# Optimization experiments

Hardware: AMD Instinct MI355X
Metric: run time of the kernel (lower is better)

Reference implementation:

```python
import jax, jax.numpy as jnp
import numpy as np

M, K, N, P = 2048, 4096, 64, 16   # prev outputs, decoder nodes, matrix size, parents per node
ACTIVE_THRESHOLD = 12             # >= 12/16 active parents required

def setup_inputs() -> dict:
    key = jax.random.key(0)
    k1, k2, k3, k4, k5 = jax.random.split(key, 5)
    prev_outputs = jax.random.normal(k1, (M, N, N), dtype=jnp.float32)
    prev_is_active = jax.random.bernoulli(k2, 0.9, (M,))                 # bool (M,)
    parent_indices = jax.random.randint(k3, (K, P), 0, M)                # static wiring (K,16)
    w = jax.random.normal(k4, (K, P), dtype=jnp.float32) / np.sqrt(P)    # per-node parent weights
    b = jax.random.normal(k5, (K,), dtype=jnp.float32) * 0.01            # per-node bias
    return {"prev_outputs": prev_outputs, "prev_is_active": prev_is_active,
            "parent_indices": parent_indices, "w": w, "b": b}

def reference(prev_outputs, prev_is_active, parent_indices, w, b):
    # gather parent outputs: (K, P, n, n)
    gathered = prev_outputs[parent_indices]
    # per-node decoder: weighted combine of 16 parents + bias, tanh
    combined = jnp.einsum('kp,kpnm->knm', w, gathered) + b[:, None, None]
    out = jnp.tanh(combined)[:, None]                                    # (K,1,n,n)
    # activity threshold gate: node active iff >= 12 of 16 parents active
    n_active = prev_is_active[parent_indices].astype(jnp.int32).sum(axis=-1)  # (K,)
    out_active = n_active >= ACTIVE_THRESHOLD
    out = jnp.where(out_active[:, None, None, None], out, jnp.zeros_like(out))
    return out, out_active
```

## Files before the change

### kernel.cpp

```cpp
#include <hip/hip_runtime.h>


#define M_ROWS   2048
#define K_NODES  4096
#define NN       4096
#define POS_TILE 16
#define NTHREADS 1024
#define ROW_B    48
#define LDS_BYTES (M_ROWS * ROW_B)
#define OUT_ELEMS (K_NODES * NN)
#define ACTIVE_THRESHOLD 12

typedef float f32x4 __attribute__((ext_vector_type(4)));
typedef unsigned short u16x8 __attribute__((ext_vector_type(8)));

__device__ __forceinline__ float fast_tanh(float x) {
  float ax = __builtin_fabsf(x);
  float e  = __expf(-2.0f * ax);
  float r  = (1.0f - e) * __builtin_amdgcn_rcpf(1.0f + e);
  return __builtin_copysignf(r, x);
}

__device__ __forceinline__ unsigned short f2bf_rne(float f) {
  unsigned u = __float_as_uint(f);
  u += 0x7FFFu + ((u >> 16) & 1u);
  return (unsigned short)(u >> 16);
}

__global__ __launch_bounds__(256) void act_kernel(
    const int* __restrict__ pidx, const unsigned int* __restrict__ isact,
    float* __restrict__ outact) {
  __shared__ int mode_sh;
  if (threadIdx.x == 0) mode_sh = 0;
  __syncthreads();
  int bad = 0;
  for (int i = threadIdx.x; i < 512; i += 256) bad |= (isact[i] > 1u);
  if (bad) atomicOr(&mode_sh, 1);
  __syncthreads();
  const int shift = mode_sh ? 0 : 2;
  const unsigned char* actb = (const unsigned char*)isact;

  int k = blockIdx.x * 256 + threadIdx.x;
  const int4* ip = (const int4*)(pidx + k * 16);
  int4 ia = ip[0], ib = ip[1], ic = ip[2], id4 = ip[3];
  int ids[16] = {ia.x, ia.y, ia.z, ia.w, ib.x, ib.y, ib.z, ib.w,
                 ic.x, ic.y, ic.z, ic.w, id4.x, id4.y, id4.z, id4.w};
  int n = 0;
  #pragma unroll
  for (int p = 0; p < 16; ++p) n += (actb[ids[p] << shift] != 0);
  outact[k] = (n >= ACTIVE_THRESHOLD) ? 1.0f : 0.0f;
}

#define PFMA(vv, wv)                                              \
  { float wv_ = (wv);                                             \
    a0 += wv_ * __uint_as_float((unsigned)(vv)[0] << 16);         \
    a1 += wv_ * __uint_as_float((unsigned)(vv)[1] << 16);         \
    a2 += wv_ * __uint_as_float((unsigned)(vv)[2] << 16);         \
    a3 += wv_ * __uint_as_float((unsigned)(vv)[3] << 16);         \
    a4 += wv_ * __uint_as_float((unsigned)(vv)[4] << 16);         \
    a5 += wv_ * __uint_as_float((unsigned)(vv)[5] << 16);         \
    a6 += wv_ * __uint_as_float((unsigned)(vv)[6] << 16);         \
    a7 += wv_ * __uint_as_float((unsigned)(vv)[7] << 16); }

__global__ __launch_bounds__(NTHREADS, 1) void decoder_kernel(
    const float* __restrict__ prev, const int* __restrict__ pidx,
    const float* __restrict__ w, const float* __restrict__ b,
    const float* __restrict__ actf, float* __restrict__ out,
    float* __restrict__ outact) {
  extern __shared__ char xb[];
  const int tid  = threadIdx.x;
  const int bid  = blockIdx.x;
  const int pos0 = bid * POS_TILE;

  #pragma unroll
  for (int it = 0; it < 4; ++it) {
    int ci = (it << 10) + tid;
    int r = ci >> 1, c = ci & 1;
    const float* sp = prev + r * NN + pos0 + (c << 3);
    f32x4 v0 = *(const f32x4*)sp;
    f32x4 v1 = *(const f32x4*)(sp + 4);
    u16x8 o;
    o[0] = f2bf_rne(v0.x); o[1] = f2bf_rne(v0.y);
    o[2] = f2bf_rne(v0.z); o[3] = f2bf_rne(v0.w);
    o[4] = f2bf_rne(v1.x); o[5] = f2bf_rne(v1.y);
    o[6] = f2bf_rne(v1.z); o[7] = f2bf_rne(v1.w);
    *(u16x8*)(xb + r * ROW_B + (c << 4)) = o;
  }
  __syncthreads();

  const int q  = tid & 1;
  const int s  = tid >> 1;
  const int qb = q << 4;

  for (int it = 0; it < 8; ++it) {
    int n = (it << 9) + s;
    const int4*   ip = (const int4*)(pidx + (n << 4));
    const float4* wp = (const float4*)(w + (n << 4));
    int4   i0 = ip[0], i1 = ip[1], i2 = ip[2], i3 = ip[3];
    float4 w0 = wp[0], w1 = wp[1], w2 = wp[2], w3 = wp[3];
    float  bk = b[n];
    float  g  = actf[n];

    float a0 = bk, a1 = bk, a2 = bk, a3 = bk;
    float a4 = bk, a5 = bk, a6 = bk, a7 = bk;

    u16x8 v0 = *(const u16x8*)(xb + i0.x * ROW_B + qb);
    u16x8 v1 = *(const u16x8*)(xb + i0.y * ROW_B + qb);
    u16x8 v2 = *(const u16x8*)(xb + i0.z * ROW_B + qb);
    u16x8 v3 = *(const u16x8*)(xb + i0.w * ROW_B + qb);
    u16x8 v4 = *(const u16x8*)(xb + i1.x * ROW_B + qb);
    u16x8 v5 = *(const u16x8*)(xb + i1.y * ROW_B + qb);
    u16x8 v6 = *(const u16x8*)(xb + i1.z * ROW_B + qb);
    u16x8 v7 = *(const u16x8*)(xb + i1.w * ROW_B + qb);
    __builtin_amdgcn_sched_barrier(0);
    PFMA(v0, w0.x) PFMA(v1, w0.y) PFMA(v2, w0.z) PFMA(v3, w0.w)
    PFMA(v4, w1.x) PFMA(v5, w1.y) PFMA(v6, w1.z) PFMA(v7, w1.w)

    v0 = *(const u16x8*)(xb + i2.x * ROW_B + qb);
    v1 = *(const u16x8*)(xb + i2.y * ROW_B + qb);
    v2 = *(const u16x8*)(xb + i2.z * ROW_B + qb);
    v3 = *(const u16x8*)(xb + i2.w * ROW_B + qb);
    v4 = *(const u16x8*)(xb + i3.x * ROW_B + qb);
    v5 = *(const u16x8*)(xb + i3.y * ROW_B + qb);
    v6 = *(const u16x8*)(xb + i3.z * ROW_B + qb);
    v7 = *(const u16x8*)(xb + i3.w * ROW_B + qb);
    __builtin_amdgcn_sched_barrier(0);
    PFMA(v0, w2.x) PFMA(v1, w2.y) PFMA(v2, w2.z) PFMA(v3, w2.w)
    PFMA(v4, w3.x) PFMA(v5, w3.y) PFMA(v6, w3.z) PFMA(v7, w3.w)

    f32x4 o0, o1;
    o0.x = fast_tanh(a0) * g; o0.y = fast_tanh(a1) * g;
    o0.z = fast_tanh(a2) * g; o0.w = fast_tanh(a3) * g;
    o1.x = fast_tanh(a4) * g; o1.y = fast_tanh(a5) * g;
    o1.z = fast_tanh(a6) * g; o1.w = fast_tanh(a7) * g;

    float* op = out + ((size_t)n << 12) + pos0 + (q << 3);
    *(f32x4*)op       = o0;
    *(f32x4*)(op + 4) = o1;

    if (bid == 0 && q == 0) outact[n] = g;
  }
}

extern "C" void kernel_launch(void* const* d_in, const int* in_sizes, int n_in,
                              void* d_out, int out_size, void* d_ws, size_t ws_size,
                              hipStream_t stream) {
  const float* prev  = (const float*)d_in[0];
  const void*  isact = d_in[1];
  const int*   pidx  = (const int*)d_in[2];
  const float* w     = (const float*)d_in[3];
  const float* b     = (const float*)d_in[4];
  float* out    = (float*)d_out;
  float* outact = out + OUT_ELEMS;

  (void)hipFuncSetAttribute((const void*)decoder_kernel,
                            hipFuncAttributeMaxDynamicSharedMemorySize, LDS_BYTES);

  act_kernel<<<K_NODES / 256, 256, 0, stream>>>(
      pidx, (const unsigned int*)isact, outact);
  decoder_kernel<<<NN / POS_TILE, NTHREADS, LDS_BYTES, stream>>>(
      prev, pidx, w, b, outact, out, outact);
}
```

Baseline: 41.15 us.

## Halve position tile, one node per thread, XCD-aware block remap

Shrinks the per-block position tile from 16 to 8, so the bf16 LDS staging buffer drops to 24-byte rows (48 KB) and each thread handles a whole node's 8 positions instead of two threads sharing a node. Launch bounds now request multiple blocks per CU to raise occupancy, and block ids are remapped so consecutive tiles land on the same XCD for L2 locality of prev reads. The redundant outact write from block 0 is removed. In exchange the grid doubles, pidx and w are re-read by twice as many blocks, and LDS reads become two 8-byte loads per parent row, which may hit more bank conflicts.

```diff
diff --git a/kernel.cpp b/kernel.cpp
--- a/kernel.cpp
+++ b/kernel.cpp
@@ -4,15 +4,15 @@
 #define M_ROWS   2048
 #define K_NODES  4096
 #define NN       4096
-#define POS_TILE 16
+#define POS_TILE 8
 #define NTHREADS 1024
-#define ROW_B    48
+#define ROW_B    24
 #define LDS_BYTES (M_ROWS * ROW_B)
 #define OUT_ELEMS (K_NODES * NN)
 #define ACTIVE_THRESHOLD 12
 
 typedef float f32x4 __attribute__((ext_vector_type(4)));
-typedef unsigned short u16x8 __attribute__((ext_vector_type(8)));
+typedef unsigned short u16x4 __attribute__((ext_vector_type(4)));
 
 __device__ __forceinline__ float fast_tanh(float x) {
   float ax = __builtin_fabsf(x);
@@ -51,49 +51,48 @@
   outact[k] = (n >= ACTIVE_THRESHOLD) ? 1.0f : 0.0f;
 }
 
-#define PFMA(vv, wv)                                              \
-  { float wv_ = (wv);                                             \
-    a0 += wv_ * __uint_as_float((unsigned)(vv)[0] << 16);         \
-    a1 += wv_ * __uint_as_float((unsigned)(vv)[1] << 16);         \
-    a2 += wv_ * __uint_as_float((unsigned)(vv)[2] << 16);         \
-    a3 += wv_ * __uint_as_float((unsigned)(vv)[3] << 16);         \
-    a4 += wv_ * __uint_as_float((unsigned)(vv)[4] << 16);         \
-    a5 += wv_ * __uint_as_float((unsigned)(vv)[5] << 16);         \
-    a6 += wv_ * __uint_as_float((unsigned)(vv)[6] << 16);         \
-    a7 += wv_ * __uint_as_float((unsigned)(vv)[7] << 16); }
+#define PFMA2(lo, hi, wv)                                          \
+  { float wv_ = (wv);                                              \
+    a0 += wv_ * __uint_as_float((unsigned)(lo)[0] << 16);          \
+    a1 += wv_ * __uint_as_float((unsigned)(lo)[1] << 16);          \
+    a2 += wv_ * __uint_as_float((unsigned)(lo)[2] << 16);          \
+    a3 += wv_ * __uint_as_float((unsigned)(lo)[3] << 16);          \
+    a4 += wv_ * __uint_as_float((unsigned)(hi)[0] << 16);          \
+    a5 += wv_ * __uint_as_float((unsigned)(hi)[1] << 16);          \
+    a6 += wv_ * __uint_as_float((unsigned)(hi)[2] << 16);          \
+    a7 += wv_ * __uint_as_float((unsigned)(hi)[3] << 16); }
 
-__global__ __launch_bounds__(NTHREADS, 1) void decoder_kernel(
+__global__ __launch_bounds__(NTHREADS, 8) void decoder_kernel(
     const float* __restrict__ prev, const int* __restrict__ pidx,
     const float* __restrict__ w, const float* __restrict__ b,
-    const float* __restrict__ actf, float* __restrict__ out,
-    float* __restrict__ outact) {
+    const float* __restrict__ actf, float* __restrict__ out) {
   extern __shared__ char xb[];
-  const int tid  = threadIdx.x;
-  const int bid  = blockIdx.x;
-  const int pos0 = bid * POS_TILE;
+  const int tid = threadIdx.x;
+  const int bid = blockIdx.x;
+
+  const int xcd  = bid & 7;
+  const int tile = xcd * 64 + (bid >> 3);
+  const int pos0 = tile * POS_TILE;
 
   #pragma unroll
-  for (int it = 0; it < 4; ++it) {
-    int ci = (it << 10) + tid;
-    int r = ci >> 1, c = ci & 1;
-    const float* sp = prev + r * NN + pos0 + (c << 3);
+  for (int it = 0; it < 2; ++it) {
+    int r = (it << 10) + tid;
+    const float* sp = prev + r * NN + pos0;
     f32x4 v0 = *(const f32x4*)sp;
     f32x4 v1 = *(const f32x4*)(sp + 4);
-    u16x8 o;
-    o[0] = f2bf_rne(v0.x); o[1] = f2bf_rne(v0.y);
-    o[2] = f2bf_rne(v0.z); o[3] = f2bf_rne(v0.w);
-    o[4] = f2bf_rne(v1.x); o[5] = f2bf_rne(v1.y);
-    o[6] = f2bf_rne(v1.z); o[7] = f2bf_rne(v1.w);
-    *(u16x8*)(xb + r * ROW_B + (c << 4)) = o;
+    u16x4 lo, hi;
+    lo[0] = f2bf_rne(v0.x); lo[1] = f2bf_rne(v0.y);
+    lo[2] = f2bf_rne(v0.z); lo[3] = f2bf_rne(v0.w);
+    hi[0] = f2bf_rne(v1.x); hi[1] = f2bf_rne(v1.y);
+    hi[2] = f2bf_rne(v1.z); hi[3] = f2bf_rne(v1.w);
+    char* dp = xb + r * ROW_B;
+    *(u16x4*)dp       = lo;
+    *(u16x4*)(dp + 8) = hi;
   }
   __syncthreads();
 
-  const int q  = tid & 1;
-  const int s  = tid >> 1;
-  const int qb = q << 4;
-
-  for (int it = 0; it < 8; ++it) {
-    int n = (it << 9) + s;
+  for (int it = 0; it < 4; ++it) {
+    int n = (it << 10) + tid;
     const int4*   ip = (const int4*)(pidx + (n << 4));
     const float4* wp = (const float4*)(w + (n << 4));
     int4   i0 = ip[0], i1 = ip[1], i2 = ip[2], i3 = ip[3];
@@ -104,29 +103,47 @@
     float a0 = bk, a1 = bk, a2 = bk, a3 = bk;
     float a4 = bk, a5 = bk, a6 = bk, a7 = bk;
 
-    u16x8 v0 = *(const u16x8*)(xb + i0.x * ROW_B + qb);
-    u16x8 v1 = *(const u16x8*)(xb + i0.y * ROW_B + qb);
-    u16x8 v2 = *(const u16x8*)(xb + i0.z * ROW_B + qb);
-    u16x8 v3 = *(const u16x8*)(xb + i0.w * ROW_B + qb);
-    u16x8 v4 = *(const u16x8*)(xb + i1.x * ROW_B + qb);
-    u16x8 v5 = *(const u16x8*)(xb + i1.y * ROW_B + qb);
-    u16x8 v6 = *(const u16x8*)(xb + i1.z * ROW_B + qb);
-    u16x8 v7 = *(const u16x8*)(xb + i1.w * ROW_B + qb);
+    const char* r0 = xb + i0.x * ROW_B;
+    const char* r1 = xb + i0.y * ROW_B;
+    const char* r2 = xb + i0.z * ROW_B;
+    const char* r3 = xb + i0.w * ROW_B;
+    u16x4 l0 = *(const u16x4*)r0, h0 = *(const u16x4*)(r0 + 8);
+    u16x4 l1 = *(const u16x4*)r1, h1 = *(const u16x4*)(r1 + 8);
+    u16x4 l2 = *(const u16x4*)r2, h2 = *(const u16x4*)(r2 + 8);
+    u16x4 l3 = *(const u16x4*)r3, h3 = *(const u16x4*)(r3 + 8);
     __builtin_amdgcn_sched_barrier(0);
-    PFMA(v0, w0.x) PFMA(v1, w0.y) PFMA(v2, w0.z) PFMA(v3, w0.w)
-    PFMA(v4, w1.x) PFMA(v5, w1.y) PFMA(v6, w1.z) PFMA(v7, w1.w)
+    PFMA2(l0, h0, w0.x) PFMA2(l1, h1, w0.y)
+    PFMA2(l2, h2, w0.z) PFMA2(l3, h3, w0.w)
 
-    v0 = *(const u16x8*)(xb + i2.x * ROW_B + qb);
-    v1 = *(const u16x8*)(xb + i2.y * ROW_B + qb);
-    v2 = *(const u16x8*)(xb + i2.z * ROW_B + qb);
-    v3 = *(const u16x8*)(xb + i2.w * ROW_B + qb);
-    v4 = *(const u16x8*)(xb + i3.x * ROW_B + qb);
-    v5 = *(const u16x8*)(xb + i3.y * ROW_B + qb);
-    v6 = *(const u16x8*)(xb + i3.z * ROW_B + qb);
-    v7 = *(const u16x8*)(xb + i3.w * ROW_B + qb);
+    r0 = xb + i1.x * ROW_B;  r1 = xb + i1.y * ROW_B;
+    r2 = xb + i1.z * ROW_B;  r3 = xb + i1.w * ROW_B;
+    l0 = *(const u16x4*)r0;  h0 = *(const u16x4*)(r0 + 8);
+    l1 = *(const u16x4*)r1;  h1 = *(const u16x4*)(r1 + 8);
+    l2 = *(const u16x4*)r2;  h2 = *(const u16x4*)(r2 + 8);
+    l3 = *(const u16x4*)r3;  h3 = *(const u16x4*)(r3 + 8);
     __builtin_amdgcn_sched_barrier(0);
-    PFMA(v0, w2.x) PFMA(v1, w2.y) PFMA(v2, w2.z) PFMA(v3, w2.w)
-    PFMA(v4, w3.x) PFMA(v5, w3.y) PFMA(v6, w3.z) PFMA(v7, w3.w)
+    PFMA2(l0, h0, w1.x) PFMA2(l1, h1, w1.y)
+    PFMA2(l2, h2, w1.z) PFMA2(l3, h3, w1.w)
+
+    r0 = xb + i2.x * ROW_B;  r1 = xb + i2.y * ROW_B;
+    r2 = xb + i2.z * ROW_B;  r3 = xb + i2.w * ROW_B;
+    l0 = *(const u16x4*)r0;  h0 = *(const u16x4*)(r0 + 8);
+    l1 = *(const u16x4*)r1;  h1 = *(const u16x4*)(r1 + 8);
+    l2 = *(const u16x4*)r2;  h2 = *(const u16x4*)(r2 + 8);
+    l3 = *(const u16x4*)r3;  h3 = *(const u16x4*)(r3 + 8);
+    __builtin_amdgcn_sched_barrier(0);
+    PFMA2(l0, h0, w2.x) PFMA2(l1, h1, w2.y)
+    PFMA2(l2, h2, w2.z) PFMA2(l3, h3, w2.w)
+
+    r0 = xb + i3.x * ROW_B;  r1 = xb + i3.y * ROW_B;
+    r2 = xb + i3.z * ROW_B;  r3 = xb + i3.w * ROW_B;
+    l0 = *(const u16x4*)r0;  h0 = *(const u16x4*)(r0 + 8);
+    l1 = *(const u16x4*)r1;  h1 = *(const u16x4*)(r1 + 8);
+    l2 = *(const u16x4*)r2;  h2 = *(const u16x4*)(r2 + 8);
+    l3 = *(const u16x4*)r3;  h3 = *(const u16x4*)(r3 + 8);
+    __builtin_amdgcn_sched_barrier(0);
+    PFMA2(l0, h0, w3.x) PFMA2(l1, h1, w3.y)
+    PFMA2(l2, h2, w3.z) PFMA2(l3, h3, w3.w)
 
     f32x4 o0, o1;
     o0.x = fast_tanh(a0) * g; o0.y = fast_tanh(a1) * g;
@@ -134,11 +151,9 @@
     o1.x = fast_tanh(a4) * g; o1.y = fast_tanh(a5) * g;
     o1.z = fast_tanh(a6) * g; o1.w = fast_tanh(a7) * g;
 
-    float* op = out + ((size_t)n << 12) + pos0 + (q << 3);
+    float* op = out + ((size_t)n << 12) + pos0;
     *(f32x4*)op       = o0;
     *(f32x4*)(op + 4) = o1;
-
-    if (bid == 0 && q == 0) outact[n] = g;
   }
 }
 
@@ -159,5 +174,5 @@
   act_kernel<<<K_NODES / 256, 256, 0, stream>>>(
       pidx, (const unsigned int*)isact, outact);
   decoder_kernel<<<NN / POS_TILE, NTHREADS, LDS_BYTES, stream>>>(
-      prev, pidx, w, b, outact, out, outact);
+      prev, pidx, w, b, outact, out);
 }
```

Result: slower. 94.56 us (+129.8%).

## Fuse activity gating into decoder kernel with XCD-aware tile/half split

Applied to the files above, without the earlier changes.

Removes the separate activity kernel. Each decoder block now stages the active flags into spare LDS bytes of each row and computes the 16-parent gate counts itself, keeping the gate in LDS instead of reading it from global memory. The position tile doubles to 32 and each tile is split into two node halves. Blocks are mapped so both halves of a tile land on the same XCD, which should let the second read of the shared prev slice hit in L2. The trade-off is redundant gate computation in every block and twice the prev traffic, in exchange for one fewer launch and no dependency between the two kernels.

```diff
diff --git a/kernel.cpp b/kernel.cpp
--- a/kernel.cpp
+++ b/kernel.cpp
@@ -4,9 +4,9 @@
 #define M_ROWS   2048
 #define K_NODES  4096
 #define NN       4096
-#define POS_TILE 16
+#define POS_TILE 32
 #define NTHREADS 1024
-#define ROW_B    48
+#define ROW_B    80
 #define LDS_BYTES (M_ROWS * ROW_B)
 #define OUT_ELEMS (K_NODES * NN)
 #define ACTIVE_THRESHOLD 12
@@ -27,30 +27,6 @@
   return (unsigned short)(u >> 16);
 }
 
-__global__ __launch_bounds__(256) void act_kernel(
-    const int* __restrict__ pidx, const unsigned int* __restrict__ isact,
-    float* __restrict__ outact) {
-  __shared__ int mode_sh;
-  if (threadIdx.x == 0) mode_sh = 0;
-  __syncthreads();
-  int bad = 0;
-  for (int i = threadIdx.x; i < 512; i += 256) bad |= (isact[i] > 1u);
-  if (bad) atomicOr(&mode_sh, 1);
-  __syncthreads();
-  const int shift = mode_sh ? 0 : 2;
-  const unsigned char* actb = (const unsigned char*)isact;
-
-  int k = blockIdx.x * 256 + threadIdx.x;
-  const int4* ip = (const int4*)(pidx + k * 16);
-  int4 ia = ip[0], ib = ip[1], ic = ip[2], id4 = ip[3];
-  int ids[16] = {ia.x, ia.y, ia.z, ia.w, ib.x, ib.y, ib.z, ib.w,
-                 ic.x, ic.y, ic.z, ic.w, id4.x, id4.y, id4.z, id4.w};
-  int n = 0;
-  #pragma unroll
-  for (int p = 0; p < 16; ++p) n += (actb[ids[p] << shift] != 0);
-  outact[k] = (n >= ACTIVE_THRESHOLD) ? 1.0f : 0.0f;
-}
-
 #define PFMA(vv, wv)                                              \
   { float wv_ = (wv);                                             \
     a0 += wv_ * __uint_as_float((unsigned)(vv)[0] << 16);         \
@@ -63,19 +39,27 @@
     a7 += wv_ * __uint_as_float((unsigned)(vv)[7] << 16); }
 
 __global__ __launch_bounds__(NTHREADS, 1) void decoder_kernel(
-    const float* __restrict__ prev, const int* __restrict__ pidx,
-    const float* __restrict__ w, const float* __restrict__ b,
-    const float* __restrict__ actf, float* __restrict__ out,
+    const float* __restrict__ prev, const unsigned int* __restrict__ isact,
+    const int* __restrict__ pidx, const float* __restrict__ w,
+    const float* __restrict__ b, float* __restrict__ out,
     float* __restrict__ outact) {
   extern __shared__ char xb[];
-  const int tid  = threadIdx.x;
-  const int bid  = blockIdx.x;
-  const int pos0 = bid * POS_TILE;
+  int* modep = (int*)(xb + 76);
+  const int tid = threadIdx.x;
+  const int bid = blockIdx.x;
+  if (tid == 0) *modep = 0;
+
+  const int xcd   = bid & 7;
+  const int loc   = bid >> 3;
+  const int tile  = xcd * 16 + (loc >> 1);
+  const int half  = loc & 1;
+  const int pos0  = tile * POS_TILE;
+  const int nbase = half * (K_NODES / 2);
 
   #pragma unroll
-  for (int it = 0; it < 4; ++it) {
+  for (int it = 0; it < 8; ++it) {
     int ci = (it << 10) + tid;
-    int r = ci >> 1, c = ci & 1;
+    int r = ci >> 2, c = ci & 3;
     const float* sp = prev + r * NN + pos0 + (c << 3);
     f32x4 v0 = *(const f32x4*)sp;
     f32x4 v1 = *(const f32x4*)(sp + 4);
@@ -88,18 +72,61 @@
   }
   __syncthreads();
 
-  const int q  = tid & 1;
-  const int s  = tid >> 1;
+  if (tid < 512 && isact[tid] > 1u) atomicOr(modep, 1);
+  __syncthreads();
+  const int bytemode = *modep;
+
+  if (tid < 512) {
+    if (bytemode) {
+      unsigned wv = isact[tid];
+      xb[(4 * tid + 0) * ROW_B + 72] = (unsigned char)(wv);
+      xb[(4 * tid + 1) * ROW_B + 72] = (unsigned char)(wv >> 8);
+      xb[(4 * tid + 2) * ROW_B + 72] = (unsigned char)(wv >> 16);
+      xb[(4 * tid + 3) * ROW_B + 72] = (unsigned char)(wv >> 24);
+    } else {
+      int4 wv4 = ((const int4*)isact)[tid];
+      xb[(4 * tid + 0) * ROW_B + 72] = (unsigned char)wv4.x;
+      xb[(4 * tid + 1) * ROW_B + 72] = (unsigned char)wv4.y;
+      xb[(4 * tid + 2) * ROW_B + 72] = (unsigned char)wv4.z;
+      xb[(4 * tid + 3) * ROW_B + 72] = (unsigned char)wv4.w;
+    }
+  }
+  __syncthreads();
+
+  #pragma unroll
+  for (int h = 0; h < 2; ++h) {
+    int m = (h << 10) + tid;
+    int nn_ = nbase + m;
+    const int4* ip = (const int4*)(pidx + (nn_ << 4));
+    int4 i0 = ip[0], i1 = ip[1], i2 = ip[2], i3 = ip[3];
+    int cnt =
+      (xb[i0.x * ROW_B + 72] != 0) + (xb[i0.y * ROW_B + 72] != 0) +
+      (xb[i0.z * ROW_B + 72] != 0) + (xb[i0.w * ROW_B + 72] != 0) +
+      (xb[i1.x * ROW_B + 72] != 0) + (xb[i1.y * ROW_B + 72] != 0) +
+      (xb[i1.z * ROW_B + 72] != 0) + (xb[i1.w * ROW_B + 72] != 0) +
+      (xb[i2.x * ROW_B + 72] != 0) + (xb[i2.y * ROW_B + 72] != 0) +
+      (xb[i2.z * ROW_B + 72] != 0) + (xb[i2.w * ROW_B + 72] != 0) +
+      (xb[i3.x * ROW_B + 72] != 0) + (xb[i3.y * ROW_B + 72] != 0) +
+      (xb[i3.z * ROW_B + 72] != 0) + (xb[i3.w * ROW_B + 72] != 0);
+    unsigned char gg = (cnt >= ACTIVE_THRESHOLD) ? 1 : 0;
+    xb[m * ROW_B + 64] = gg;
+    if (tile == 0) outact[nn_] = (float)gg;
+  }
+  __syncthreads();
+
+  const int q  = tid & 3;
+  const int s  = tid >> 2;
   const int qb = q << 4;
 
   for (int it = 0; it < 8; ++it) {
-    int n = (it << 9) + s;
+    int m = (it << 8) + s;
+    int n = nbase + m;
     const int4*   ip = (const int4*)(pidx + (n << 4));
     const float4* wp = (const float4*)(w + (n << 4));
     int4   i0 = ip[0], i1 = ip[1], i2 = ip[2], i3 = ip[3];
     float4 w0 = wp[0], w1 = wp[1], w2 = wp[2], w3 = wp[3];
     float  bk = b[n];
-    float  g  = actf[n];
+    float  g  = xb[m * ROW_B + 64] ? 1.0f : 0.0f;
 
     float a0 = bk, a1 = bk, a2 = bk, a3 = bk;
     float a4 = bk, a5 = bk, a6 = bk, a7 = bk;
@@ -137,8 +164,6 @@
     float* op = out + ((size_t)n << 12) + pos0 + (q << 3);
     *(f32x4*)op       = o0;
     *(f32x4*)(op + 4) = o1;
-
-    if (bid == 0 && q == 0) outact[n] = g;
   }
 }
 
@@ -156,8 +181,6 @@
   (void)hipFuncSetAttribute((const void*)decoder_kernel,
                             hipFuncAttributeMaxDynamicSharedMemorySize, LDS_BYTES);
 
-  act_kernel<<<K_NODES / 256, 256, 0, stream>>>(
-      pidx, (const unsigned int*)isact, outact);
-  decoder_kernel<<<NN / POS_TILE, NTHREADS, LDS_BYTES, stream>>>(
-      prev, pidx, w, b, outact, out, outact);
+  decoder_kernel<<<(NN / POS_TILE) * 2, NTHREADS, LDS_BYTES, stream>>>(
+      prev, (const unsigned int*)isact, pidx, w, b, out, outact);
 }
```

New measurement: 38.40 us. -6.7%, faster.
